# Optimization experiments

Measured on AMD Instinct MI355X. Metric: run time of the kernel, lower is better.

## Reference

```python
import jax, jax.numpy as jnp
import numpy as np

N_NODES = 20000
N_EDGES = 320000
IN_DIM = 512
HID = 256
N_GRAPHS = 256


def setup_inputs() -> dict:
    key = jax.random.key(0)
    ks = jax.random.split(key, 7)
    x = jax.random.normal(ks[0], (N_NODES, IN_DIM), dtype=jnp.float32)
    edge_index = jax.random.randint(ks[1], (2, N_EDGES), 0, N_NODES, dtype=jnp.int64)
    batch = jnp.sort(jax.random.randint(ks[2], (N_NODES,), 0, N_GRAPHS, dtype=jnp.int64))
    W = jax.random.normal(ks[3], (IN_DIM, HID), dtype=jnp.float32) * (1.0 / np.sqrt(IN_DIM))
    b = jax.random.normal(ks[4], (HID,), dtype=jnp.float32) * 0.02
    lin_w = jax.random.normal(ks[5], (HID, 1), dtype=jnp.float32) * (1.0 / np.sqrt(HID))
    lin_b = jax.random.normal(ks[6], (1,), dtype=jnp.float32) * 0.02
    return {"x": x, "edge_index": edge_index, "batch": batch,
            "W": W, "b": b, "lin_w": lin_w, "lin_b": lin_b}


def reference(x, edge_index, batch, W, b, lin_w, lin_b):
    N = x.shape[0]
    # --- GCNConv: add self-loops, symmetric normalization ---
    loop = jnp.arange(N, dtype=edge_index.dtype)
    src = jnp.concatenate([edge_index[0], loop])   # [E+N]
    dst = jnp.concatenate([edge_index[1], loop])   # [E+N]
    deg = jax.ops.segment_sum(jnp.ones_like(dst, dtype=x.dtype), dst, num_segments=N)
    dinv = jnp.where(deg > 0, jax.lax.rsqrt(deg), 0.0)          # [N]
    norm = dinv[src] * dinv[dst]                                 # [E+N]
    h = x @ W                                                    # [N, HID] dense GEMM
    msgs = h[src] * norm[:, None]                                # gather + scale
    agg = jax.ops.segment_sum(msgs, dst, num_segments=N) + b     # scatter-add
    xr = jax.nn.relu(agg)                                        # [N, HID]
    # --- global_mean_pool over graph ids ---
    sums = jax.ops.segment_sum(xr, batch, num_segments=N_GRAPHS)             # [G, HID]
    counts = jax.ops.segment_sum(jnp.ones((N,), dtype=x.dtype), batch, num_segments=N_GRAPHS)
    pooled = sums / jnp.maximum(counts, 1.0)[:, None]
    # --- linear head + sigmoid ---
    out = jax.nn.sigmoid(pooled @ lin_w + lin_b)                 # [G, 1]
    return out.reshape(-1)
```

## Files before the change

### kernel.cpp

```cpp
#include <hip/hip_runtime.h>
#include <hip/hip_bf16.h>
#include <cstdint>

typedef __attribute__((ext_vector_type(8))) _Float16 half8;
typedef __attribute__((ext_vector_type(4))) _Float16 half4;
typedef __attribute__((ext_vector_type(2))) float f32x2;
typedef __attribute__((ext_vector_type(4))) float f32x4;

#define N_NODES 20000
#define N_EDGES 320000
#define IN_DIM 512
#define HID 256
#define N_GRAPHS 256
#define NPB 8
#define DSTRIDE 64

#define PREP_WBLK 16
#define PREP_EBLK (N_EDGES / 256)
#define PREP_BBLK ((N_NODES + 255) / 256)
__global__ __launch_bounds__(256) void prep_kernel(const float* __restrict__ W,
                                                   const int* __restrict__ src,
                                                   const int* __restrict__ dst,
                                                   const int* __restrict__ batch,
                                                   _Float16* __restrict__ wt,
                                                   int* __restrict__ cnt2,
                                                   int* __restrict__ csr,
                                                   int* __restrict__ counts) {
    int b = blockIdx.x, t = threadIdx.x;
    if (b < PREP_WBLK) {
        __shared__ _Float16 tile[32 * 256];
        int k0 = b * 32;
        const float4* wp = reinterpret_cast<const float4*>(W + (size_t)k0 * HID);
#pragma unroll
        for (int i = 0; i < 8; ++i) {
            float4 v = wp[i * 256 + t];
            int flat = (i * 256 + t) * 4;
            int kk = flat >> 8, n = flat & 255;
            half4 hv;
            hv[0] = (_Float16)v.x; hv[1] = (_Float16)v.y;
            hv[2] = (_Float16)v.z; hv[3] = (_Float16)v.w;
            *reinterpret_cast<half4*>(&tile[kk * 256 + n]) = hv;
        }
        __syncthreads();
        alignas(16) _Float16 vals[32];
#pragma unroll
        for (int kk = 0; kk < 32; ++kk) vals[kk] = tile[kk * 256 + t];
        uint4* op = reinterpret_cast<uint4*>((char*)wt + (size_t)t * 1024 + (size_t)k0 * 2);
        const uint4* vp = reinterpret_cast<const uint4*>(vals);
#pragma unroll
        for (int j = 0; j < 4; ++j) op[j] = vp[j];
    } else if (b < PREP_WBLK + PREP_EBLK) {
        int e = (b - PREP_WBLK) * 256 + t;
        int d = dst[e];
        int slot = atomicAdd(&cnt2[d], 1);
        if (slot < DSTRIDE) csr[d * DSTRIDE + slot] = src[e];
    } else {
        int i = (b - PREP_WBLK - PREP_EBLK) * 256 + t;
        if (i < N_NODES) atomicAdd(&counts[batch[i]], 1);
    }
}

#define GEMM_BLOCKS ((N_NODES + 63) / 64)

#define LOADA(Sa, Sb, Sc, Sd, k0) do { const float* ap_ = aptr + (k0); \
    Sa = *reinterpret_cast<const float4*>(ap_);         \
    Sb = *reinterpret_cast<const float4*>(ap_ + 4);     \
    Sc = *reinterpret_cast<const float4*>(ap_ + 32);    \
    Sd = *reinterpret_cast<const float4*>(ap_ + 36); } while (0)

#define PACKA(Sa, Sb, Sc, Sd) do { \
    a0[0]=(_Float16)Sa.x; a0[1]=(_Float16)Sa.y; a0[2]=(_Float16)Sa.z; a0[3]=(_Float16)Sa.w; \
    a0[4]=(_Float16)Sb.x; a0[5]=(_Float16)Sb.y; a0[6]=(_Float16)Sb.z; a0[7]=(_Float16)Sb.w; \
    a1[0]=(_Float16)Sc.x; a1[1]=(_Float16)Sc.y; a1[2]=(_Float16)Sc.z; a1[3]=(_Float16)Sc.w; \
    a1[4]=(_Float16)Sd.x; a1[5]=(_Float16)Sd.y; a1[6]=(_Float16)Sd.z; a1[7]=(_Float16)Sd.w; } while (0)

#define LOADB(s) do { const uint4* ws_ = wsrc + 8 * (s); \
    wb0=ws_[0]; wb1=ws_[1]; wb2=ws_[2]; wb3=ws_[3];      \
    wb4=ws_[4]; wb5=ws_[5]; wb6=ws_[6]; wb7=ws_[7]; } while (0)

#define STAGEB(q) do { uint4* d_ = reinterpret_cast<uint4*>(myst + ((q) << 15)); \
    d_[0^tsw]=wb0; d_[1^tsw]=wb1; d_[2^tsw]=wb2; d_[3^tsw]=wb3;                  \
    d_[4^tsw]=wb4; d_[5^tsw]=wb5; d_[6^tsw]=wb6; d_[7^tsw]=wb7; } while (0)

#define KBARRIER() do { asm volatile("s_waitcnt lgkmcnt(0)" ::: "memory"); \
    __builtin_amdgcn_s_barrier(); asm volatile("" ::: "memory"); } while (0)

#define MFMASTEP(q) do { const char* rb_ = (const char*)bsl + ((q) << 15); \
    _Pragma("unroll")                                                      \
    for (int nt = 0; nt < 16; ++nt) {                                      \
        int c_ = nt * 16 + col; int cs_ = c_ & 7;                          \
        half8 bb0_ = *reinterpret_cast<const half8*>(rb_ + c_ * 128 + ((quad ^ cs_) << 4));       \
        acc[nt] = __builtin_amdgcn_mfma_f32_16x16x32_f16(a0, bb0_, acc[nt], 0, 0, 0);             \
        half8 bb1_ = *reinterpret_cast<const half8*>(rb_ + c_ * 128 + (((4 + quad) ^ cs_) << 4)); \
        acc[nt] = __builtin_amdgcn_mfma_f32_16x16x32_f16(a1, bb1_, acc[nt], 0, 0, 0);             \
    } } while (0)

__global__ __launch_bounds__(256, 2) void gemm_kernel(const float* __restrict__ x,
                                                      const _Float16* __restrict__ wt,
                                                      unsigned char* __restrict__ h8,
                                                      const int* __restrict__ cnt2) {
    __shared__ _Float16 bsl[2 * 256 * 64];
    const int K = IN_DIM;
    int t    = threadIdx.x;
    int lane = t & 63;
    int wave = t >> 6;
    int col  = lane & 15;
    int quad = lane >> 4;
    int row0 = blockIdx.x * 64 + wave * 16;

    f32x4 acc[16];
#pragma unroll
    for (int i = 0; i < 16; ++i) acc[i] = (f32x4){0.f, 0.f, 0.f, 0.f};

    int arow = row0 + col;
    if (arow >= N_NODES) arow = N_NODES - 1;
    const float* aptr = x + (size_t)arow * K + quad * 8;
    const uint4* wsrc = reinterpret_cast<const uint4*>(wt + (size_t)t * K);

    char* myst = (char*)bsl + t * 128;
    int tsw = t & 7;

    float4 sA0, sA1, sA2, sA3;
    float4 sB0, sB1, sB2, sB3;
    uint4  wb0, wb1, wb2, wb3, wb4, wb5, wb6, wb7;
    half8  a0, a1;

    LOADB(0);
    LOADA(sA0, sA1, sA2, sA3, 0);
    LOADA(sB0, sB1, sB2, sB3, 64);
    STAGEB(0);
    LOADB(1);
    KBARRIER();

#pragma unroll
    for (int it = 0; it < 4; ++it) {
        PACKA(sA0, sA1, sA2, sA3);
        if (it < 3) LOADA(sA0, sA1, sA2, sA3, (2 * it + 2) * 64);
        STAGEB(1);
        if (it < 3) LOADB(2 * it + 2);
        MFMASTEP(0);
        KBARRIER();
        PACKA(sB0, sB1, sB2, sB3);
        if (it < 3) LOADA(sB0, sB1, sB2, sB3, (2 * it + 3) * 64);
        if (it < 3) { STAGEB(0); LOADB(2 * it + 3); }
        MFMASTEP(1);
        KBARRIER();
    }

    int orow0 = row0 + quad * 4;
    float dv[4];
#pragma unroll
    for (int r = 0; r < 4; ++r) {
        int rr = orow0 + r;
        if (rr >= N_NODES) rr = N_NODES - 1;
        dv[r] = rsqrtf((float)cnt2[rr] + 1.f);
    }
#pragma unroll
    for (int nt = 0; nt < 16; ++nt) {
#pragma unroll
        for (int r = 0; r < 4; ++r) {
            int rr = orow0 + r;
            if (rr < N_NODES) {
                float v = acc[nt][r] * dv[r];
                int pk = __builtin_amdgcn_cvt_pk_fp8_f32(v, v, 0, false);
                h8[(size_t)rr * HID + nt * 16 + col] = (unsigned char)(pk & 0xff);
            }
        }
    }
}

__global__ __launch_bounds__(256, 8) void aggregate_kernel(const unsigned char* __restrict__ h8,
                                                           const float* __restrict__ bias,
                                                           const int* __restrict__ cnt2,
                                                           const int* __restrict__ csr,
                                                           const int* __restrict__ batch,
                                                           float* __restrict__ sums) {
    __shared__ float pool[NPB * HID];
    int v0  = blockIdx.x * NPB;
    int t   = threadIdx.x;
    int grp = t >> 6;
    int fl  = t & 63;
    int vg  = v0 + grp * 2;
    const float4 bf = *reinterpret_cast<const float4*>(bias + 4 * fl);

    float a0[2], a1[2], a2[2], a3[2], dvv[2];
#pragma unroll
    for (int i = 0; i < 2; ++i) {
        int v = vg + i;
        int cnt = cnt2[v]; if (cnt > DSTRIDE) cnt = DSTRIDE;
        dvv[i] = rsqrtf((float)cnt + 1.f);
        unsigned int u = *reinterpret_cast<const unsigned int*>(h8 + (size_t)v * HID + 4 * fl);
        f32x2 lo = __builtin_amdgcn_cvt_pk_f32_fp8(u, false);
        f32x2 hi = __builtin_amdgcn_cvt_pk_f32_fp8(u, true);
        float x0 = lo[0], x1 = lo[1], x2 = hi[0], x3 = hi[1];
        int ecv = csr[v * DSTRIDE + fl];
        int j = 0;
        for (; j + 4 <= cnt; j += 4) {
            int s0 = __shfl(ecv, j, 64);
            int s1 = __shfl(ecv, j + 1, 64);
            int s2 = __shfl(ecv, j + 2, 64);
            int s3 = __shfl(ecv, j + 3, 64);
            unsigned int u0 = *reinterpret_cast<const unsigned int*>(h8 + (size_t)s0 * HID + 4 * fl);
            unsigned int u1 = *reinterpret_cast<const unsigned int*>(h8 + (size_t)s1 * HID + 4 * fl);
            unsigned int u2 = *reinterpret_cast<const unsigned int*>(h8 + (size_t)s2 * HID + 4 * fl);
            unsigned int u3 = *reinterpret_cast<const unsigned int*>(h8 + (size_t)s3 * HID + 4 * fl);
            f32x2 p;
            p = __builtin_amdgcn_cvt_pk_f32_fp8(u0, false); x0 += p[0]; x1 += p[1];
            p = __builtin_amdgcn_cvt_pk_f32_fp8(u0, true);  x2 += p[0]; x3 += p[1];
            p = __builtin_amdgcn_cvt_pk_f32_fp8(u1, false); x0 += p[0]; x1 += p[1];
            p = __builtin_amdgcn_cvt_pk_f32_fp8(u1, true);  x2 += p[0]; x3 += p[1];
            p = __builtin_amdgcn_cvt_pk_f32_fp8(u2, false); x0 += p[0]; x1 += p[1];
            p = __builtin_amdgcn_cvt_pk_f32_fp8(u2, true);  x2 += p[0]; x3 += p[1];
            p = __builtin_amdgcn_cvt_pk_f32_fp8(u3, false); x0 += p[0]; x1 += p[1];
            p = __builtin_amdgcn_cvt_pk_f32_fp8(u3, true);  x2 += p[0]; x3 += p[1];
        }
        for (; j < cnt; ++j) {
            int s = __shfl(ecv, j, 64);
            unsigned int u4 = *reinterpret_cast<const unsigned int*>(h8 + (size_t)s * HID + 4 * fl);
            f32x2 p;
            p = __builtin_amdgcn_cvt_pk_f32_fp8(u4, false); x0 += p[0]; x1 += p[1];
            p = __builtin_amdgcn_cvt_pk_f32_fp8(u4, true);  x2 += p[0]; x3 += p[1];
        }
        a0[i] = x0; a1[i] = x1; a2[i] = x2; a3[i] = x3;
    }

#pragma unroll
    for (int i = 0; i < 2; ++i) {
        f32x4 r;
        r[0] = fmaxf(dvv[i] * a0[i] + bf.x, 0.f);
        r[1] = fmaxf(dvv[i] * a1[i] + bf.y, 0.f);
        r[2] = fmaxf(dvv[i] * a2[i] + bf.z, 0.f);
        r[3] = fmaxf(dvv[i] * a3[i] + bf.w, 0.f);
        *reinterpret_cast<f32x4*>(&pool[(grp * 2 + i) * HID + 4 * fl]) = r;
    }
    __syncthreads();

    float acc = 0.f;
    int cur_g = batch[v0];
#pragma unroll
    for (int i = 0; i < NPB; ++i) {
        float val = pool[i * HID + t];
        int g = batch[v0 + i];
        if (g != cur_g) {
            atomicAdd(&sums[(size_t)cur_g * HID + t], acc);
            acc = 0.f;
            cur_g = g;
        }
        acc += val;
    }
    atomicAdd(&sums[(size_t)cur_g * HID + t], acc);
}

__global__ __launch_bounds__(256) void head_kernel(const float* __restrict__ sums,
                                                   const int* __restrict__ counts,
                                                   const float* __restrict__ lin_w,
                                                   const float* __restrict__ lin_b,
                                                   float* __restrict__ out) {
    int g = blockIdx.x;
    int f = threadIdx.x;
    float c = (float)counts[g];
    if (c < 1.f) c = 1.f;
    float v = (sums[(size_t)g * HID + f] / c) * lin_w[f];
#pragma unroll
    for (int off = 32; off >= 1; off >>= 1) v += __shfl_down(v, off, 64);
    __shared__ float red[4];
    if ((f & 63) == 0) red[f >> 6] = v;
    __syncthreads();
    if (f == 0) {
        float s = red[0] + red[1] + red[2] + red[3] + lin_b[0];
        out[g] = 1.0f / (1.0f + expf(-s));
    }
}

extern "C" void kernel_launch(void* const* d_in, const int* in_sizes, int n_in,
                              void* d_out, int out_size, void* d_ws, size_t ws_size,
                              hipStream_t stream) {
    const float* x     = (const float*)d_in[0];
    const int*   edge  = (const int*)d_in[1];
    const int*   batch = (const int*)d_in[2];
    const float* W     = (const float*)d_in[3];
    const float* b     = (const float*)d_in[4];
    const float* lin_w = (const float*)d_in[5];
    const float* lin_b = (const float*)d_in[6];
    float*       out   = (float*)d_out;

    const int N = N_NODES, E = N_EDGES, G = N_GRAPHS, K = IN_DIM, H = HID;
    const int* src = edge;
    const int* dst = edge + E;

    char* p = (char*)d_ws;
    auto alloc = [&](size_t bytes) {
        char* r = p;
        p += (bytes + 255) & ~(size_t)255;
        return r;
    };
    _Float16*      wt  = (_Float16*)alloc((size_t)H * K * 2);
    unsigned char* h8  = (unsigned char*)alloc((size_t)N * H);
    int*           csr = (int*)alloc((size_t)N * DSTRIDE * 4);
    char* z0 = p;
    int*   cnt2   = (int*)alloc((size_t)N * 4);
    float* sums   = (float*)alloc((size_t)G * H * 4);
    int*   counts = (int*)alloc((size_t)G * 4);
    size_t zbytes = (size_t)(p - z0);

    hipMemsetAsync(z0, 0, zbytes, stream);

    prep_kernel<<<PREP_WBLK + PREP_EBLK + PREP_BBLK, 256, 0, stream>>>(W, src, dst, batch,
                                                                       wt, cnt2, csr, counts);
    gemm_kernel<<<GEMM_BLOCKS, 256, 0, stream>>>(x, wt, h8, cnt2);
    aggregate_kernel<<<N / NPB, 256, 0, stream>>>(h8, b, cnt2, csr, batch, sums);
    head_kernel<<<G, 256, 0, stream>>>(sums, counts, lin_w, lin_b, out);
}
```

Baseline: 171.2 us.

## Overlap CSR construction with GEMM by moving source-degree scaling into aggregation

The edge-bucketing (CSR build with atomics) moves out of the prep kernel and into extra blocks of the GEMM launch, so it runs alongside the dense GEMM. The GEMM therefore no longer depends on degree counts and stores unscaled fp8 rows. The source-side normalisation is now applied per neighbour in the aggregate kernel, which adds a gathered degree load and an rsqrt for each edge. The intent is to take the atomic CSR pass off the critical path. The cost is more gather traffic and arithmetic in aggregation, and fp8 rounding now applies before the scaling rather than after.

```diff
diff --git a/kernel.cpp b/kernel.cpp
--- a/kernel.cpp
+++ b/kernel.cpp
@@ -16,15 +16,10 @@
 #define DSTRIDE 64
 
 #define PREP_WBLK 16
-#define PREP_EBLK (N_EDGES / 256)
 #define PREP_BBLK ((N_NODES + 255) / 256)
 __global__ __launch_bounds__(256) void prep_kernel(const float* __restrict__ W,
-                                                   const int* __restrict__ src,
-                                                   const int* __restrict__ dst,
                                                    const int* __restrict__ batch,
                                                    _Float16* __restrict__ wt,
-                                                   int* __restrict__ cnt2,
-                                                   int* __restrict__ csr,
                                                    int* __restrict__ counts) {
     int b = blockIdx.x, t = threadIdx.x;
     if (b < PREP_WBLK) {
@@ -49,18 +44,14 @@
         const uint4* vp = reinterpret_cast<const uint4*>(vals);
 #pragma unroll
         for (int j = 0; j < 4; ++j) op[j] = vp[j];
-    } else if (b < PREP_WBLK + PREP_EBLK) {
-        int e = (b - PREP_WBLK) * 256 + t;
-        int d = dst[e];
-        int slot = atomicAdd(&cnt2[d], 1);
-        if (slot < DSTRIDE) csr[d * DSTRIDE + slot] = src[e];
     } else {
-        int i = (b - PREP_WBLK - PREP_EBLK) * 256 + t;
+        int i = (b - PREP_WBLK) * 256 + t;
         if (i < N_NODES) atomicAdd(&counts[batch[i]], 1);
     }
 }
 
 #define GEMM_BLOCKS ((N_NODES + 63) / 64)
+#define CSR_BLOCKS  (N_EDGES / 256)
 
 #define LOADA(Sa, Sb, Sc, Sd, k0) do { const float* ap_ = aptr + (k0); \
     Sa = *reinterpret_cast<const float4*>(ap_);         \
@@ -95,11 +86,21 @@
         acc[nt] = __builtin_amdgcn_mfma_f32_16x16x32_f16(a1, bb1_, acc[nt], 0, 0, 0);             \
     } } while (0)
 
-__global__ __launch_bounds__(256, 2) void gemm_kernel(const float* __restrict__ x,
-                                                      const _Float16* __restrict__ wt,
-                                                      unsigned char* __restrict__ h8,
-                                                      const int* __restrict__ cnt2) {
+__global__ __launch_bounds__(256, 2) void gemm_csr_kernel(const float* __restrict__ x,
+                                                          const _Float16* __restrict__ wt,
+                                                          unsigned char* __restrict__ h8,
+                                                          const int* __restrict__ src,
+                                                          const int* __restrict__ dst,
+                                                          int* __restrict__ cnt2,
+                                                          int* __restrict__ csr) {
     __shared__ _Float16 bsl[2 * 256 * 64];
+    if (blockIdx.x >= GEMM_BLOCKS) {
+        int e = (blockIdx.x - GEMM_BLOCKS) * 256 + threadIdx.x;
+        int d = dst[e];
+        int slot = atomicAdd(&cnt2[d], 1);
+        if (slot < DSTRIDE) csr[d * DSTRIDE + slot] = src[e];
+        return;
+    }
     const int K = IN_DIM;
     int t    = threadIdx.x;
     int lane = t & 63;
@@ -148,20 +149,13 @@
     }
 
     int orow0 = row0 + quad * 4;
-    float dv[4];
-#pragma unroll
-    for (int r = 0; r < 4; ++r) {
-        int rr = orow0 + r;
-        if (rr >= N_NODES) rr = N_NODES - 1;
-        dv[r] = rsqrtf((float)cnt2[rr] + 1.f);
-    }
 #pragma unroll
     for (int nt = 0; nt < 16; ++nt) {
 #pragma unroll
         for (int r = 0; r < 4; ++r) {
             int rr = orow0 + r;
             if (rr < N_NODES) {
-                float v = acc[nt][r] * dv[r];
+                float v = acc[nt][r];
                 int pk = __builtin_amdgcn_cvt_pk_fp8_f32(v, v, 0, false);
                 h8[(size_t)rr * HID + nt * 16 + col] = (unsigned char)(pk & 0xff);
             }
@@ -187,12 +181,14 @@
 #pragma unroll
     for (int i = 0; i < 2; ++i) {
         int v = vg + i;
-        int cnt = cnt2[v]; if (cnt > DSTRIDE) cnt = DSTRIDE;
-        dvv[i] = rsqrtf((float)cnt + 1.f);
+        int ctrue = cnt2[v];
+        int cnt = ctrue; if (cnt > DSTRIDE) cnt = DSTRIDE;
+        float dv = rsqrtf((float)ctrue + 1.f);
+        dvv[i] = dv;
         unsigned int u = *reinterpret_cast<const unsigned int*>(h8 + (size_t)v * HID + 4 * fl);
         f32x2 lo = __builtin_amdgcn_cvt_pk_f32_fp8(u, false);
         f32x2 hi = __builtin_amdgcn_cvt_pk_f32_fp8(u, true);
-        float x0 = lo[0], x1 = lo[1], x2 = hi[0], x3 = hi[1];
+        float x0 = dv * lo[0], x1 = dv * lo[1], x2 = dv * hi[0], x3 = dv * hi[1];
         int ecv = csr[v * DSTRIDE + fl];
         int j = 0;
         for (; j + 4 <= cnt; j += 4) {
@@ -200,26 +196,33 @@
             int s1 = __shfl(ecv, j + 1, 64);
             int s2 = __shfl(ecv, j + 2, 64);
             int s3 = __shfl(ecv, j + 3, 64);
+            int c0 = cnt2[s0], c1 = cnt2[s1], c2 = cnt2[s2], c3 = cnt2[s3];
             unsigned int u0 = *reinterpret_cast<const unsigned int*>(h8 + (size_t)s0 * HID + 4 * fl);
             unsigned int u1 = *reinterpret_cast<const unsigned int*>(h8 + (size_t)s1 * HID + 4 * fl);
             unsigned int u2 = *reinterpret_cast<const unsigned int*>(h8 + (size_t)s2 * HID + 4 * fl);
             unsigned int u3 = *reinterpret_cast<const unsigned int*>(h8 + (size_t)s3 * HID + 4 * fl);
+            float d0 = rsqrtf((float)c0 + 1.f);
+            float d1 = rsqrtf((float)c1 + 1.f);
+            float d2 = rsqrtf((float)c2 + 1.f);
+            float d3 = rsqrtf((float)c3 + 1.f);
             f32x2 p;
-            p = __builtin_amdgcn_cvt_pk_f32_fp8(u0, false); x0 += p[0]; x1 += p[1];
-            p = __builtin_amdgcn_cvt_pk_f32_fp8(u0, true);  x2 += p[0]; x3 += p[1];
-            p = __builtin_amdgcn_cvt_pk_f32_fp8(u1, false); x0 += p[0]; x1 += p[1];
-            p = __builtin_amdgcn_cvt_pk_f32_fp8(u1, true);  x2 += p[0]; x3 += p[1];
-            p = __builtin_amdgcn_cvt_pk_f32_fp8(u2, false); x0 += p[0]; x1 += p[1];
-            p = __builtin_amdgcn_cvt_pk_f32_fp8(u2, true);  x2 += p[0]; x3 += p[1];
-            p = __builtin_amdgcn_cvt_pk_f32_fp8(u3, false); x0 += p[0]; x1 += p[1];
-            p = __builtin_amdgcn_cvt_pk_f32_fp8(u3, true);  x2 += p[0]; x3 += p[1];
+            p = __builtin_amdgcn_cvt_pk_f32_fp8(u0, false); x0 += d0 * p[0]; x1 += d0 * p[1];
+            p = __builtin_amdgcn_cvt_pk_f32_fp8(u0, true);  x2 += d0 * p[0]; x3 += d0 * p[1];
+            p = __builtin_amdgcn_cvt_pk_f32_fp8(u1, false); x0 += d1 * p[0]; x1 += d1 * p[1];
+            p = __builtin_amdgcn_cvt_pk_f32_fp8(u1, true);  x2 += d1 * p[0]; x3 += d1 * p[1];
+            p = __builtin_amdgcn_cvt_pk_f32_fp8(u2, false); x0 += d2 * p[0]; x1 += d2 * p[1];
+            p = __builtin_amdgcn_cvt_pk_f32_fp8(u2, true);  x2 += d2 * p[0]; x3 += d2 * p[1];
+            p = __builtin_amdgcn_cvt_pk_f32_fp8(u3, false); x0 += d3 * p[0]; x1 += d3 * p[1];
+            p = __builtin_amdgcn_cvt_pk_f32_fp8(u3, true);  x2 += d3 * p[0]; x3 += d3 * p[1];
         }
         for (; j < cnt; ++j) {
             int s = __shfl(ecv, j, 64);
+            int c = cnt2[s];
             unsigned int u4 = *reinterpret_cast<const unsigned int*>(h8 + (size_t)s * HID + 4 * fl);
+            float ds = rsqrtf((float)c + 1.f);
             f32x2 p;
-            p = __builtin_amdgcn_cvt_pk_f32_fp8(u4, false); x0 += p[0]; x1 += p[1];
-            p = __builtin_amdgcn_cvt_pk_f32_fp8(u4, true);  x2 += p[0]; x3 += p[1];
+            p = __builtin_amdgcn_cvt_pk_f32_fp8(u4, false); x0 += ds * p[0]; x1 += ds * p[1];
+            p = __builtin_amdgcn_cvt_pk_f32_fp8(u4, true);  x2 += ds * p[0]; x3 += ds * p[1];
         }
         a0[i] = x0; a1[i] = x1; a2[i] = x2; a3[i] = x3;
     }
@@ -305,9 +308,9 @@
 
     hipMemsetAsync(z0, 0, zbytes, stream);
 
-    prep_kernel<<<PREP_WBLK + PREP_EBLK + PREP_BBLK, 256, 0, stream>>>(W, src, dst, batch,
-                                                                       wt, cnt2, csr, counts);
-    gemm_kernel<<<GEMM_BLOCKS, 256, 0, stream>>>(x, wt, h8, cnt2);
+    prep_kernel<<<PREP_WBLK + PREP_BBLK, 256, 0, stream>>>(W, batch, wt, counts);
+    gemm_csr_kernel<<<GEMM_BLOCKS + CSR_BLOCKS, 256, 0, stream>>>(x, wt, h8, src, dst,
+                                                                  cnt2, csr);
     aggregate_kernel<<<N / NPB, 256, 0, stream>>>(h8, b, cnt2, csr, batch, sums);
     head_kernel<<<G, 256, 0, stream>>>(sums, counts, lin_w, lin_b, out);
 }
```

After: 160.7 us. 1.07x faster.
